# Performance work log

Measured on AMD Instinct MI355X. Metric: run time of the kernel, lower is better.

The kernel has to match this reference:

```python
import jax, jax.numpy as jnp
import numpy as np

CONTEXT_LENGTH = 4096
INPUT_LENGTH = 1024
N_EMBED = 512
HEAD_SIZE = 64
BATCH = 8


def _prefix_causal_mask(T):
    # A=ones(IL,IL), B=zeros(IL,non), C=ones(non,IL), D=tril(non,non)
    il = INPUT_LENGTH
    non = CONTEXT_LENGTH - il
    top = jnp.concatenate([jnp.ones((il, il)), jnp.zeros((il, non))], axis=1)
    bot = jnp.concatenate([jnp.ones((non, il)), jnp.tril(jnp.ones((non, non)))], axis=1)
    E = jnp.concatenate([top, bot], axis=0)
    return E[:T, :T]


def setup_inputs() -> dict:
    key = jax.random.key(0)
    kx, kq, kk, kv = jax.random.split(key, 4)
    scale = N_EMBED ** -0.5
    return {
        "x": jax.random.normal(kx, (BATCH, CONTEXT_LENGTH, N_EMBED), dtype=jnp.float32),
        "Wq": jax.random.normal(kq, (N_EMBED, HEAD_SIZE), dtype=jnp.float32) * scale,
        "Wk": jax.random.normal(kk, (N_EMBED, HEAD_SIZE), dtype=jnp.float32) * scale,
        "Wv": jax.random.normal(kv, (N_EMBED, HEAD_SIZE), dtype=jnp.float32) * scale,
    }


def reference(x, Wq, Wk, Wv):
    B, T, C = x.shape
    q = x @ Wq  # [B,T,h]
    k = x @ Wk  # [B,T,h]
    v = x @ Wv  # [B,T,h]
    # NOTE: original scales by C**-0.5 with C = n_embed (not head_size)
    wei = jnp.einsum("bth,bsh->bts", q, k) * (C ** -0.5)  # [B,T,T]
    mask = _prefix_causal_mask(T)  # [T,T], 1 = visible
    wei = jnp.where(mask == 0, jnp.float32(-jnp.inf), wei)
    wei = jax.nn.softmax(wei, axis=-1)
    # dropout p=0.0 (eval): identity
    return jnp.einsum("bts,bsh->bth", wei, v)  # [B,T,h]
```

## Files before the change

### kernel.cpp

```cpp
#include <hip/hip_runtime.h>
#include <hip/hip_bf16.h>


typedef short short8 __attribute__((ext_vector_type(8)));
typedef float floatx4 __attribute__((ext_vector_type(4)));

static __device__ __forceinline__ unsigned short f2b(float f) {
  unsigned u = __float_as_uint(f);
  unsigned r = (u + 0x7fffu + ((u >> 16) & 1u)) >> 16;
  return (unsigned short)r;
}

static __device__ __forceinline__ unsigned pkbf(float lo, float hi) {
  __hip_bfloat162 t = __float22bfloat162_rn(make_float2(lo, hi));
  unsigned d;
  __builtin_memcpy(&d, &t, 4);
  return d;
}

union S8U {
  short8 s;
  unsigned u[4];
};

__global__ __launch_bounds__(256) void wtrans(
    const float* __restrict__ Wq, const float* __restrict__ Wk,
    const float* __restrict__ Wv, unsigned short* __restrict__ Wtf) {
  int o = blockIdx.x * 256 + threadIdx.x;
  int e = o & 7;
  int ln = (o >> 3) & 63;
  int jg = o >> 9;
  int ks = jg / 12;
  int j = jg % 12;
  int m = j >> 2;
  int n = (j & 3) * 16 + (ln & 15);
  int k = ks * 32 + (ln >> 4) * 8 + e;
  const float* W = (m == 0) ? Wq : (m == 1) ? Wk : Wv;
  Wtf[o] = f2b(W[k * 64 + n]);
}

__global__ __launch_bounds__(256, 3) void proj(
    const float* __restrict__ x, const unsigned short* __restrict__ Wtf,
    unsigned short* __restrict__ q, unsigned short* __restrict__ Kf,
    unsigned short* __restrict__ Vf) {
  __shared__ float Cc[2][12][16][17];

  const int tid = threadIdx.x;
  const int lane = tid & 63;
  const int w = tid >> 6;
  const int u = lane & 15;
  const int qd = lane >> 4;
  const int pr = w >> 1;
  const int p = w & 1;
  const int g0 = blockIdx.x * 32;

  floatx4 acc[12];
#pragma unroll
  for (int j = 0; j < 12; ++j) acc[j] = (floatx4)0.0f;

  const float* xr = x + (size_t)(g0 + pr * 16 + u) * 512;

  for (int it = 0; it < 8; ++it) {
    const int ks = p + it * 2;
    floatx4 x0 = *reinterpret_cast<const floatx4*>(&xr[ks * 32 + qd * 8]);
    floatx4 x1 = *reinterpret_cast<const floatx4*>(&xr[ks * 32 + qd * 8 + 4]);
    S8U a;
    a.u[0] = pkbf(x0[0], x0[1]);
    a.u[1] = pkbf(x0[2], x0[3]);
    a.u[2] = pkbf(x1[0], x1[1]);
    a.u[3] = pkbf(x1[2], x1[3]);
#pragma unroll
    for (int j = 0; j < 12; ++j) {
      short8 bfr = *reinterpret_cast<const short8*>(&Wtf[(size_t)(ks * 12 + j) * 512 + lane * 8]);
      acc[j] = __builtin_amdgcn_mfma_f32_16x16x32_bf16(a.s, bfr, acc[j], 0, 0, 0);
    }
  }

  if (p == 1) {
#pragma unroll
    for (int j = 0; j < 12; ++j)
#pragma unroll
      for (int r = 0; r < 4; ++r)
        Cc[pr][j][qd * 4 + r][u] = acc[j][r];
  }
  __syncthreads();
  if (p == 0) {
#pragma unroll
    for (int j = 0; j < 12; ++j)
#pragma unroll
      for (int r = 0; r < 4; ++r)
        acc[j][r] += Cc[pr][j][qd * 4 + r][u];

    const int rbase = g0 + pr * 16;
    const int b = rbase >> 12;
    const int t = rbase & 4095;
    const int kt = t >> 6;
    const int sb = ((blockIdx.x & 1) << 1) + pr;
    const int sp = blockIdx.x & 1;
    unsigned short* kfb = Kf + ((size_t)(b * 64 + kt)) * 4096;
    unsigned short* vfb = Vf + ((size_t)(b * 64 + kt)) * 4096;

#pragma unroll
    for (int j = 0; j < 4; ++j)
#pragma unroll
      for (int r = 0; r < 4; ++r) {
        q[(size_t)(rbase + qd * 4 + r) * 64 + j * 16 + u] = f2b(acc[j][r]);
        {
          int kh = j >> 1;
          int qd_f = ((j & 1) << 1) + (u >> 3);
          kfb[(size_t)(kh * 4 + sb) * 512 + (qd_f * 16 + (qd * 4 + r)) * 8 + (u & 7)] =
              f2b(acc[4 + j][r]);
        }
        {
          int qd_f = pr * 2 + (qd >> 1);
          int e = ((qd & 1) << 2) + r;
          vfb[(size_t)(sp * 4 + j) * 512 + (qd_f * 16 + u) * 8 + e] = f2b(acc[8 + j][r]);
        }
      }
  }
}

__global__ __launch_bounds__(256, 2) void attn(
    const unsigned short* __restrict__ q, const unsigned short* __restrict__ Kf,
    const unsigned short* __restrict__ Vf, float* __restrict__ out) {
  __shared__ unsigned Pb[4][4][64][4];
  __shared__ float OcA[64][68];
  __shared__ float OcB[64][68];
  __shared__ float Lc[4][64];

  const int tid = threadIdx.x;
  const int lane = tid & 63;
  const int w = tid >> 6;
  const int u = lane & 15;
  const int qd = lane >> 4;

  const int bx = blockIdx.x;
  const int b = bx & 7;
  const int i = bx >> 3;
  const int qt = (i < 32) ? i : (95 - i);
  const int g0 = qt * 64;

  const unsigned short* qp = q + (size_t)b * 4096 * 64;
  const unsigned short* kfp = Kf + (size_t)b * 64 * 4096;
  const unsigned short* vfp = Vf + (size_t)b * 64 * 4096;

  short8 qB[4][2];
#pragma unroll
  for (int nb = 0; nb < 4; ++nb)
#pragma unroll
    for (int kh = 0; kh < 2; ++kh)
      qB[nb][kh] = *reinterpret_cast<const short8*>(
          &qp[(size_t)(g0 + nb * 16 + u) * 64 + kh * 32 + qd * 8]);

  floatx4 OT[4][4];
#pragma unroll
  for (int mb = 0; mb < 4; ++mb)
#pragma unroll
    for (int nb = 0; nb < 4; ++nb) OT[mb][nb] = (floatx4)0.0f;
  float L[4] = {0.f, 0.f, 0.f, 0.f};

  const float cexp = 0.04419417382415922f * 1.4426950408889634f;
  const int ktmax = (qt < 16) ? 15 : qt;

  for (int kt = w; kt <= ktmax; kt += 4) {
    const unsigned short* kb = kfp + (size_t)kt * 4096;
    const unsigned short* vb = vfp + (size_t)kt * 4096;
    short8 kA[8];
#pragma unroll
    for (int f = 0; f < 8; ++f)
      kA[f] = *reinterpret_cast<const short8*>(&kb[(size_t)f * 512 + lane * 8]);
    const bool diag = (qt >= 16) && (kt == qt);

#pragma unroll
    for (int sp = 0; sp < 2; ++sp) {
      short8 vA[4];
#pragma unroll
      for (int mb = 0; mb < 4; ++mb)
        vA[mb] = *reinterpret_cast<const short8*>(
            &vb[(size_t)(sp * 4 + mb) * 512 + lane * 8]);

      floatx4 ST[2][4];
#pragma unroll
      for (int sbb = 0; sbb < 2; ++sbb)
#pragma unroll
        for (int nb = 0; nb < 4; ++nb) ST[sbb][nb] = (floatx4)0.0f;
#pragma unroll
      for (int kh = 0; kh < 2; ++kh)
#pragma unroll
        for (int sbb = 0; sbb < 2; ++sbb)
#pragma unroll
          for (int nb = 0; nb < 4; ++nb)
            ST[sbb][nb] = __builtin_amdgcn_mfma_f32_16x16x32_bf16(
                kA[kh * 4 + sp * 2 + sbb], qB[nb][kh], ST[sbb][nb], 0, 0, 0);

      if (diag) {
#pragma unroll
        for (int sbb = 0; sbb < 2; ++sbb)
#pragma unroll
          for (int nb = 0; nb < 4; ++nb)
#pragma unroll
            for (int r = 0; r < 4; ++r) {
              int sl = (sp * 2 + sbb) * 16 + qd * 4 + r;
              int qr = nb * 16 + u;
              if (sl > qr) ST[sbb][nb][r] = -__builtin_inff();
            }
      }

#pragma unroll
      for (int sbb = 0; sbb < 2; ++sbb)
#pragma unroll
        for (int nb = 0; nb < 4; ++nb) {
#pragma unroll
          for (int r = 0; r < 4; ++r)
            ST[sbb][nb][r] = __builtin_amdgcn_exp2f(ST[sbb][nb][r] * cexp);
          L[nb] += (ST[sbb][nb][0] + ST[sbb][nb][1]) + (ST[sbb][nb][2] + ST[sbb][nb][3]);
          unsigned lo = pkbf(ST[sbb][nb][0], ST[sbb][nb][1]);
          unsigned hi = pkbf(ST[sbb][nb][2], ST[sbb][nb][3]);
          int dl = (sbb * 2 + (qd >> 1)) * 16 + u;
          int d0 = (qd & 1) * 2;
          *reinterpret_cast<uint2*>(&Pb[w][nb][dl][d0]) = make_uint2(lo, hi);
        }

#pragma unroll
      for (int nb = 0; nb < 4; ++nb) {
        short8 pB = *reinterpret_cast<const short8*>(&Pb[w][nb][lane][0]);
#pragma unroll
        for (int mb = 0; mb < 4; ++mb)
          OT[mb][nb] = __builtin_amdgcn_mfma_f32_16x16x32_bf16(vA[mb], pB, OT[mb][nb], 0, 0, 0);
      }
    }
  }

#pragma unroll
  for (int nb = 0; nb < 4; ++nb) {
    L[nb] += __shfl_xor(L[nb], 16);
    L[nb] += __shfl_xor(L[nb], 32);
  }
  if (lane < 16) {
#pragma unroll
    for (int nb = 0; nb < 4; ++nb) Lc[w][nb * 16 + lane] = L[nb];
  }

  if (w == 1) {
#pragma unroll
    for (int mb = 0; mb < 4; ++mb)
#pragma unroll
      for (int nb = 0; nb < 4; ++nb)
        *reinterpret_cast<floatx4*>(&OcA[nb * 16 + u][mb * 16 + qd * 4]) = OT[mb][nb];
  }
  if (w == 3) {
#pragma unroll
    for (int mb = 0; mb < 4; ++mb)
#pragma unroll
      for (int nb = 0; nb < 4; ++nb)
        *reinterpret_cast<floatx4*>(&OcB[nb * 16 + u][mb * 16 + qd * 4]) = OT[mb][nb];
  }
  __syncthreads();
  if (w == 0) {
#pragma unroll
    for (int mb = 0; mb < 4; ++mb)
#pragma unroll
      for (int nb = 0; nb < 4; ++nb)
        OT[mb][nb] += *reinterpret_cast<const floatx4*>(&OcA[nb * 16 + u][mb * 16 + qd * 4]);
  }
  if (w == 2) {
#pragma unroll
    for (int mb = 0; mb < 4; ++mb)
#pragma unroll
      for (int nb = 0; nb < 4; ++nb) {
        OT[mb][nb] += *reinterpret_cast<const floatx4*>(&OcB[nb * 16 + u][mb * 16 + qd * 4]);
        *reinterpret_cast<floatx4*>(&OcB[nb * 16 + u][mb * 16 + qd * 4]) = OT[mb][nb];
      }
  }
  __syncthreads();
  if (w == 0) {
#pragma unroll
    for (int mb = 0; mb < 4; ++mb)
#pragma unroll
      for (int nb = 0; nb < 4; ++nb) {
        OT[mb][nb] += *reinterpret_cast<const floatx4*>(&OcB[nb * 16 + u][mb * 16 + qd * 4]);
        *reinterpret_cast<floatx4*>(&OcA[nb * 16 + u][mb * 16 + qd * 4]) = OT[mb][nb];
      }
  }
  __syncthreads();

  {
    int qr = tid >> 2;
    int h0 = (tid & 3) * 16;
    float Ltot = (Lc[0][qr] + Lc[1][qr]) + (Lc[2][qr] + Lc[3][qr]);
    float inv = 1.0f / Ltot;
    float* op = out + ((size_t)b * 4096 + g0 + qr) * 64 + h0;
#pragma unroll
    for (int c = 0; c < 4; ++c) {
      floatx4 v = *reinterpret_cast<const floatx4*>(&OcA[qr][h0 + c * 4]);
      v *= inv;
      *reinterpret_cast<floatx4*>(&op[c * 4]) = v;
    }
  }
}

extern "C" void kernel_launch(void* const* d_in, const int* in_sizes, int n_in,
                              void* d_out, int out_size, void* d_ws, size_t ws_size,
                              hipStream_t stream) {
  const float* x  = (const float*)d_in[0];
  const float* Wq = (const float*)d_in[1];
  const float* Wk = (const float*)d_in[2];
  const float* Wv = (const float*)d_in[3];

  unsigned short* ws = (unsigned short*)d_ws;
  unsigned short* Wtf = ws;
  unsigned short* qb = ws + 131072;
  unsigned short* kf = qb + 2097152;
  unsigned short* vf = kf + 2097152;

  wtrans<<<384, 256, 0, stream>>>(Wq, Wk, Wv, Wtf);
  proj<<<1024, 256, 0, stream>>>(x, Wtf, qb, kf, vf);
  attn<<<512, 256, 0, stream>>>(qb, kf, vf, (float*)d_out);
}
```

Before: 146.9 us.

## Split attention query tiles in half, union shared memory, fold softmax scale into Q

Each attention block now handles 32 query rows instead of 64, doubling the grid to 1024 blocks and raising launch bounds to 4 blocks per CU. Shared memory for P staging and output reduction is unioned to cut LDS usage, and K fragments are loaded per sub-block to reduce register pressure. The softmax scale (times log2 e) is folded into Q during projection, removing a multiply per score. This trades more occupancy and parallelism for K/V reloads per half-tile, and rounding the pre-scaled Q to bf16 slightly changes numerics.

```diff
diff --git a/kernel.cpp b/kernel.cpp
--- a/kernel.cpp
+++ b/kernel.cpp
@@ -91,6 +91,7 @@
       for (int r = 0; r < 4; ++r)
         acc[j][r] += Cc[pr][j][qd * 4 + r][u];
 
+    const float cexp = 0.04419417382415922f * 1.4426950408889634f;
     const int rbase = g0 + pr * 16;
     const int b = rbase >> 12;
     const int t = rbase & 4095;
@@ -104,7 +105,7 @@
     for (int j = 0; j < 4; ++j)
 #pragma unroll
       for (int r = 0; r < 4; ++r) {
-        q[(size_t)(rbase + qd * 4 + r) * 64 + j * 16 + u] = f2b(acc[j][r]);
+        q[(size_t)(rbase + qd * 4 + r) * 64 + j * 16 + u] = f2b(acc[j][r] * cexp);
         {
           int kh = j >> 1;
           int qd_f = ((j & 1) << 1) + (u >> 3);
@@ -120,13 +121,14 @@
   }
 }
 
-__global__ __launch_bounds__(256, 2) void attn(
+__global__ __launch_bounds__(256, 4) void attn(
     const unsigned short* __restrict__ q, const unsigned short* __restrict__ Kf,
     const unsigned short* __restrict__ Vf, float* __restrict__ out) {
-  __shared__ unsigned Pb[4][4][64][4];
-  __shared__ float OcA[64][68];
-  __shared__ float OcB[64][68];
-  __shared__ float Lc[4][64];
+  __shared__ union {
+    unsigned Pb[4][2][64][4];
+    struct { float A[32][68]; float B[32][68]; } Oc;
+  } sm;
+  __shared__ float Lc[4][32];
 
   const int tid = threadIdx.x;
   const int lane = tid & 63;
@@ -135,40 +137,39 @@
   const int qd = lane >> 4;
 
   const int bx = blockIdx.x;
-  const int b = bx & 7;
-  const int i = bx >> 3;
-  const int qt = (i < 32) ? i : (95 - i);
+  const int s4 = bx & 3;
+  const int m = bx >> 2;
+  const int b = m >> 5;
+  const int u0 = m & 31;
+  const int qt = (s4 & 1) ? (63 - u0) : u0;
+  const int rh = s4 >> 1;
   const int g0 = qt * 64;
+  const int r0 = rh * 32;
 
   const unsigned short* qp = q + (size_t)b * 4096 * 64;
   const unsigned short* kfp = Kf + (size_t)b * 64 * 4096;
   const unsigned short* vfp = Vf + (size_t)b * 64 * 4096;
 
-  short8 qB[4][2];
-#pragma unroll
-  for (int nb = 0; nb < 4; ++nb)
+  short8 qB[2][2];
+#pragma unroll
+  for (int nb = 0; nb < 2; ++nb)
 #pragma unroll
     for (int kh = 0; kh < 2; ++kh)
       qB[nb][kh] = *reinterpret_cast<const short8*>(
-          &qp[(size_t)(g0 + nb * 16 + u) * 64 + kh * 32 + qd * 8]);
-
-  floatx4 OT[4][4];
+          &qp[(size_t)(g0 + r0 + nb * 16 + u) * 64 + kh * 32 + qd * 8]);
+
+  floatx4 OT[4][2];
 #pragma unroll
   for (int mb = 0; mb < 4; ++mb)
 #pragma unroll
-    for (int nb = 0; nb < 4; ++nb) OT[mb][nb] = (floatx4)0.0f;
-  float L[4] = {0.f, 0.f, 0.f, 0.f};
-
-  const float cexp = 0.04419417382415922f * 1.4426950408889634f;
+    for (int nb = 0; nb < 2; ++nb) OT[mb][nb] = (floatx4)0.0f;
+  float L[2] = {0.f, 0.f};
+
   const int ktmax = (qt < 16) ? 15 : qt;
 
   for (int kt = w; kt <= ktmax; kt += 4) {
     const unsigned short* kb = kfp + (size_t)kt * 4096;
     const unsigned short* vb = vfp + (size_t)kt * 4096;
-    short8 kA[8];
-#pragma unroll
-    for (int f = 0; f < 8; ++f)
-      kA[f] = *reinterpret_cast<const short8*>(&kb[(size_t)f * 512 + lane * 8]);
     const bool diag = (qt >= 16) && (kt == qt);
 
 #pragma unroll
@@ -179,51 +180,50 @@
         vA[mb] = *reinterpret_cast<const short8*>(
             &vb[(size_t)(sp * 4 + mb) * 512 + lane * 8]);
 
-      floatx4 ST[2][4];
-#pragma unroll
-      for (int sbb = 0; sbb < 2; ++sbb)
-#pragma unroll
-        for (int nb = 0; nb < 4; ++nb) ST[sbb][nb] = (floatx4)0.0f;
-#pragma unroll
-      for (int kh = 0; kh < 2; ++kh)
-#pragma unroll
-        for (int sbb = 0; sbb < 2; ++sbb)
-#pragma unroll
-          for (int nb = 0; nb < 4; ++nb)
-            ST[sbb][nb] = __builtin_amdgcn_mfma_f32_16x16x32_bf16(
-                kA[kh * 4 + sp * 2 + sbb], qB[nb][kh], ST[sbb][nb], 0, 0, 0);
-
-      if (diag) {
-#pragma unroll
-        for (int sbb = 0; sbb < 2; ++sbb)
-#pragma unroll
-          for (int nb = 0; nb < 4; ++nb)
+#pragma unroll
+      for (int sbb = 0; sbb < 2; ++sbb) {
+        short8 kA0 = *reinterpret_cast<const short8*>(
+            &kb[(size_t)(0 * 4 + sp * 2 + sbb) * 512 + lane * 8]);
+        short8 kA1 = *reinterpret_cast<const short8*>(
+            &kb[(size_t)(1 * 4 + sp * 2 + sbb) * 512 + lane * 8]);
+
+        floatx4 ST[2];
+#pragma unroll
+        for (int nb = 0; nb < 2; ++nb) ST[nb] = (floatx4)0.0f;
+#pragma unroll
+        for (int nb = 0; nb < 2; ++nb) {
+          ST[nb] = __builtin_amdgcn_mfma_f32_16x16x32_bf16(kA0, qB[nb][0], ST[nb], 0, 0, 0);
+          ST[nb] = __builtin_amdgcn_mfma_f32_16x16x32_bf16(kA1, qB[nb][1], ST[nb], 0, 0, 0);
+        }
+
+        if (diag) {
+#pragma unroll
+          for (int nb = 0; nb < 2; ++nb)
 #pragma unroll
             for (int r = 0; r < 4; ++r) {
               int sl = (sp * 2 + sbb) * 16 + qd * 4 + r;
-              int qr = nb * 16 + u;
-              if (sl > qr) ST[sbb][nb][r] = -__builtin_inff();
+              int qr = r0 + nb * 16 + u;
+              if (sl > qr) ST[nb][r] = -__builtin_inff();
             }
-      }
-
-#pragma unroll
-      for (int sbb = 0; sbb < 2; ++sbb)
-#pragma unroll
-        for (int nb = 0; nb < 4; ++nb) {
+        }
+
+#pragma unroll
+        for (int nb = 0; nb < 2; ++nb) {
 #pragma unroll
           for (int r = 0; r < 4; ++r)
-            ST[sbb][nb][r] = __builtin_amdgcn_exp2f(ST[sbb][nb][r] * cexp);
-          L[nb] += (ST[sbb][nb][0] + ST[sbb][nb][1]) + (ST[sbb][nb][2] + ST[sbb][nb][3]);
-          unsigned lo = pkbf(ST[sbb][nb][0], ST[sbb][nb][1]);
-          unsigned hi = pkbf(ST[sbb][nb][2], ST[sbb][nb][3]);
+            ST[nb][r] = __builtin_amdgcn_exp2f(ST[nb][r]);
+          L[nb] += (ST[nb][0] + ST[nb][1]) + (ST[nb][2] + ST[nb][3]);
+          unsigned lo = pkbf(ST[nb][0], ST[nb][1]);
+          unsigned hi = pkbf(ST[nb][2], ST[nb][3]);
           int dl = (sbb * 2 + (qd >> 1)) * 16 + u;
           int d0 = (qd & 1) * 2;
-          *reinterpret_cast<uint2*>(&Pb[w][nb][dl][d0]) = make_uint2(lo, hi);
-        }
-
-#pragma unroll
-      for (int nb = 0; nb < 4; ++nb) {
-        short8 pB = *reinterpret_cast<const short8*>(&Pb[w][nb][lane][0]);
+          *reinterpret_cast<uint2*>(&sm.Pb[w][nb][dl][d0]) = make_uint2(lo, hi);
+        }
+      }
+
+#pragma unroll
+      for (int nb = 0; nb < 2; ++nb) {
+        short8 pB = *reinterpret_cast<const short8*>(&sm.Pb[w][nb][lane][0]);
 #pragma unroll
         for (int mb = 0; mb < 4; ++mb)
           OT[mb][nb] = __builtin_amdgcn_mfma_f32_16x16x32_bf16(vA[mb], pB, OT[mb][nb], 0, 0, 0);
@@ -232,44 +232,45 @@
   }
 
 #pragma unroll
-  for (int nb = 0; nb < 4; ++nb) {
+  for (int nb = 0; nb < 2; ++nb) {
     L[nb] += __shfl_xor(L[nb], 16);
     L[nb] += __shfl_xor(L[nb], 32);
   }
   if (lane < 16) {
 #pragma unroll
-    for (int nb = 0; nb < 4; ++nb) Lc[w][nb * 16 + lane] = L[nb];
-  }
+    for (int nb = 0; nb < 2; ++nb) Lc[w][nb * 16 + lane] = L[nb];
+  }
+  __syncthreads();
 
   if (w == 1) {
 #pragma unroll
     for (int mb = 0; mb < 4; ++mb)
 #pragma unroll
-      for (int nb = 0; nb < 4; ++nb)
-        *reinterpret_cast<floatx4*>(&OcA[nb * 16 + u][mb * 16 + qd * 4]) = OT[mb][nb];
+      for (int nb = 0; nb < 2; ++nb)
+        *reinterpret_cast<floatx4*>(&sm.Oc.A[nb * 16 + u][mb * 16 + qd * 4]) = OT[mb][nb];
   }
   if (w == 3) {
 #pragma unroll
     for (int mb = 0; mb < 4; ++mb)
 #pragma unroll
-      for (int nb = 0; nb < 4; ++nb)
-        *reinterpret_cast<floatx4*>(&OcB[nb * 16 + u][mb * 16 + qd * 4]) = OT[mb][nb];
+      for (int nb = 0; nb < 2; ++nb)
+        *reinterpret_cast<floatx4*>(&sm.Oc.B[nb * 16 + u][mb * 16 + qd * 4]) = OT[mb][nb];
   }
   __syncthreads();
   if (w == 0) {
 #pragma unroll
     for (int mb = 0; mb < 4; ++mb)
 #pragma unroll
-      for (int nb = 0; nb < 4; ++nb)
-        OT[mb][nb] += *reinterpret_cast<const floatx4*>(&OcA[nb * 16 + u][mb * 16 + qd * 4]);
+      for (int nb = 0; nb < 2; ++nb)
+        OT[mb][nb] += *reinterpret_cast<const floatx4*>(&sm.Oc.A[nb * 16 + u][mb * 16 + qd * 4]);
   }
   if (w == 2) {
 #pragma unroll
     for (int mb = 0; mb < 4; ++mb)
 #pragma unroll
-      for (int nb = 0; nb < 4; ++nb) {
-        OT[mb][nb] += *reinterpret_cast<const floatx4*>(&OcB[nb * 16 + u][mb * 16 + qd * 4]);
-        *reinterpret_cast<floatx4*>(&OcB[nb * 16 + u][mb * 16 + qd * 4]) = OT[mb][nb];
+      for (int nb = 0; nb < 2; ++nb) {
+        OT[mb][nb] += *reinterpret_cast<const floatx4*>(&sm.Oc.B[nb * 16 + u][mb * 16 + qd * 4]);
+        *reinterpret_cast<floatx4*>(&sm.Oc.B[nb * 16 + u][mb * 16 + qd * 4]) = OT[mb][nb];
       }
   }
   __syncthreads();
@@ -277,25 +278,25 @@
 #pragma unroll
     for (int mb = 0; mb < 4; ++mb)
 #pragma unroll
-      for (int nb = 0; nb < 4; ++nb) {
-        OT[mb][nb] += *reinterpret_cast<const floatx4*>(&OcB[nb * 16 + u][mb * 16 + qd * 4]);
-        *reinterpret_cast<floatx4*>(&OcA[nb * 16 + u][mb * 16 + qd * 4]) = OT[mb][nb];
+      for (int nb = 0; nb < 2; ++nb) {
+        OT[mb][nb] += *reinterpret_cast<const floatx4*>(&sm.Oc.B[nb * 16 + u][mb * 16 + qd * 4]);
+        *reinterpret_cast<floatx4*>(&sm.Oc.A[nb * 16 + u][mb * 16 + qd * 4]) = OT[mb][nb];
       }
   }
   __syncthreads();
 
   {
-    int qr = tid >> 2;
-    int h0 = (tid & 3) * 16;
+    int qr = tid >> 3;
+    int h0 = (tid & 7) * 8;
     float Ltot = (Lc[0][qr] + Lc[1][qr]) + (Lc[2][qr] + Lc[3][qr]);
     float inv = 1.0f / Ltot;
-    float* op = out + ((size_t)b * 4096 + g0 + qr) * 64 + h0;
-#pragma unroll
-    for (int c = 0; c < 4; ++c) {
-      floatx4 v = *reinterpret_cast<const floatx4*>(&OcA[qr][h0 + c * 4]);
-      v *= inv;
-      *reinterpret_cast<floatx4*>(&op[c * 4]) = v;
-    }
+    float* op = out + ((size_t)b * 4096 + g0 + r0 + qr) * 64 + h0;
+    floatx4 v0 = *reinterpret_cast<const floatx4*>(&sm.Oc.A[qr][h0]);
+    floatx4 v1 = *reinterpret_cast<const floatx4*>(&sm.Oc.A[qr][h0 + 4]);
+    v0 *= inv;
+    v1 *= inv;
+    *reinterpret_cast<floatx4*>(&op[0]) = v0;
+    *reinterpret_cast<floatx4*>(&op[4]) = v1;
   }
 }
 
@@ -315,5 +316,5 @@
 
   wtrans<<<384, 256, 0, stream>>>(Wq, Wk, Wv, Wtf);
   proj<<<1024, 256, 0, stream>>>(x, Wtf, qb, kf, vf);
-  attn<<<512, 256, 0, stream>>>(qb, kf, vf, (float*)d_out);
-}
+  attn<<<1024, 256, 0, stream>>>(qb, kf, vf, (float*)d_out);
+}
```

New measurement: 159.9 us. 8.9% more time.
